# Kernel tuning notes

Measured on AMD Instinct MI355X. Metric: run time of the kernel, lower is better.

## Reference

```python
import jax, jax.numpy as jnp
import numpy as np

B, S, D, H, F = 4, 1024, 2048, 16, 8192
HD = D // H  # head dim = 128
EPS = 1e-5


def layer_norm(x, w, b):
    mu = jnp.mean(x, axis=-1, keepdims=True)
    var = jnp.mean(jnp.square(x - mu), axis=-1, keepdims=True)
    return (x - mu) * jax.lax.rsqrt(var + EPS) * w + b


def setup_inputs() -> dict:
    key = jax.random.key(0)
    ks = jax.random.split(key, 12)
    s = 0.02  # realistic init scale for weights
    return {
        "x": jax.random.normal(ks[0], (B, S, D), jnp.float32),
        "attention_mask": jnp.zeros((B, 1, 1, S), jnp.float32),
        "wq": jax.random.normal(ks[1], (D, D), jnp.float32) * s,
        "bq": jax.random.normal(ks[2], (D,), jnp.float32) * s,
        "wk": jax.random.normal(ks[3], (D, D), jnp.float32) * s,
        "bk": jax.random.normal(ks[4], (D,), jnp.float32) * s,
        "wv": jax.random.normal(ks[5], (D, D), jnp.float32) * s,
        "bv": jax.random.normal(ks[6], (D,), jnp.float32) * s,
        "wo": jax.random.normal(ks[7], (D, D), jnp.float32) * s,
        "bo": jax.random.normal(ks[8], (D,), jnp.float32) * s,
        "ln1_w": jnp.ones((D,), jnp.float32),
        "ln1_b": jnp.zeros((D,), jnp.float32),
        "wi": jax.random.normal(ks[9], (F, D), jnp.float32) * s,
        "bi": jax.random.normal(ks[10], (F,), jnp.float32) * s,
        "wo2": jax.random.normal(ks[11], (D, F), jnp.float32) * s,
        "bo2": jnp.zeros((D,), jnp.float32),
        "ln2_w": jnp.ones((D,), jnp.float32),
        "ln2_b": jnp.zeros((D,), jnp.float32),
    }


def reference(x, attention_mask, wq, bq, wk, bk, wv, bv, wo, bo,
              ln1_w, ln1_b, wi, bi, wo2, bo2, ln2_w, ln2_b):
    # --- self attention ---
    q = (jnp.einsum('bsd,ed->bse', x, wq) + bq).reshape(B, S, H, HD).transpose(0, 2, 1, 3)
    k = (jnp.einsum('bsd,ed->bse', x, wk) + bk).reshape(B, S, H, HD).transpose(0, 2, 1, 3)
    v = (jnp.einsum('bsd,ed->bse', x, wv) + bv).reshape(B, S, H, HD).transpose(0, 2, 1, 3)
    scores = jnp.einsum('bhqd,bhkd->bhqk', q, k) / jnp.sqrt(jnp.float32(HD))
    scores = scores + attention_mask  # additive mask, broadcast over heads/query
    probs = jax.nn.softmax(scores, axis=-1)
    ctx = jnp.einsum('bhqk,bhkd->bhqd', probs, v)
    ctx = ctx.transpose(0, 2, 1, 3).reshape(B, S, D)
    # --- attention output: dense + bias + residual + LayerNorm ---
    attn_out = layer_norm(jnp.einsum('bsd,ed->bse', ctx, wo) + bo + x, ln1_w, ln1_b)
    # --- FFN: intermediate dense + bias, GELU, output dense + bias + residual + LN ---
    inter = jnp.einsum('bsd,fd->bsf', attn_out, wi) + bi
    h = jax.nn.gelu(inter, approximate=False)
    out = layer_norm(jnp.einsum('bsf,df->bsd', h, wo2) + bo2 + attn_out, ln2_w, ln2_b)
    return out
```

## Files before the change

### kernel.cpp

```cpp
#include <hip/hip_runtime.h>
#include <hip/hip_bf16.h>
#include <cstdint>
#include <cstddef>

typedef __attribute__((ext_vector_type(8))) short short8;
typedef __attribute__((ext_vector_type(4))) float f32x4;

#define DEV static __device__ __forceinline__

constexpr int kS = 1024, kD = 2048, kH = 16, kHD = 128, kF = 8192;
constexpr int kM = 4096;
constexpr float kEPS = 1e-5f;

constexpr size_t SZ_DD   = (size_t)kD * kD * 2;
constexpr size_t SZ_FD   = (size_t)kF * kD * 2;
constexpr size_t SZ_MD16 = (size_t)kM * kD * 2;
constexpr size_t SZ_MD32 = (size_t)kM * kD * 4;
constexpr size_t OFF_WQ  = 0;
constexpr size_t OFF_WK  = OFF_WQ + SZ_DD;
constexpr size_t OFF_WV  = OFF_WK + SZ_DD;
constexpr size_t OFF_WO  = OFF_WV + SZ_DD;
constexpr size_t OFF_WI  = OFF_WO + SZ_DD;
constexpr size_t OFF_WO2 = OFF_WI + SZ_FD;
constexpr size_t OFF_XB  = OFF_WO2 + SZ_FD;
constexpr size_t OFF_Q   = OFF_XB + SZ_MD16;
constexpr size_t OFF_K   = OFF_Q + SZ_MD16;
constexpr size_t OFF_V   = OFF_K + SZ_MD16;
constexpr size_t OFF_H   = OFF_XB;
constexpr size_t OFF_CTX = OFF_V + SZ_MD16;
constexpr size_t OFF_Y1  = OFF_CTX + SZ_MD16;
constexpr size_t OFF_A1B = OFF_Y1 + SZ_MD32;
constexpr size_t OFF_Y2  = OFF_A1B + SZ_MD16;
constexpr size_t WS_NEED = OFF_Y2 + SZ_MD32;

DEV void gload16(const void* g, void* l) {
  __builtin_amdgcn_global_load_lds(
      (const __attribute__((address_space(1))) unsigned int*)g,
      (__attribute__((address_space(3))) unsigned int*)l, 16, 0, 0);
}

__global__ void cvt_bf16(const float* __restrict__ in, __hip_bfloat16* __restrict__ out, int n4) {
  int stride = gridDim.x * blockDim.x;
  for (int i = blockIdx.x * blockDim.x + threadIdx.x; i < n4; i += stride) {
    float4 v = reinterpret_cast<const float4*>(in)[i];
    union { ushort4 u; __hip_bfloat16 h[4]; } o;
    o.h[0] = __float2bfloat16(v.x);
    o.h[1] = __float2bfloat16(v.y);
    o.h[2] = __float2bfloat16(v.z);
    o.h[3] = __float2bfloat16(v.w);
    reinterpret_cast<ushort4*>(out)[i] = o.u;
  }
}

template <int MODE>
__global__ __launch_bounds__(512, 2)
void gemm256(const __hip_bfloat16* __restrict__ A,
             const __hip_bfloat16* __restrict__ Bt,
             const float* __restrict__ bias,
             float* __restrict__ out0, float* __restrict__ out1,
             void* __restrict__ outb,
             int M, int N, int K, int kLen) {
  __shared__ __align__(16) char lds[131072];
  const int tid = threadIdx.x;
  const int lane = tid & 63, w = tid >> 6;
  const int wm = w >> 2, wn = w & 3;
  const int lg = lane >> 4, lr = lane & 15;
  const int gy = M >> 8, gx = N >> 8;
  const int nwg = gridDim.x, orig = blockIdx.x;
  const int l = (orig & 7) * (nwg >> 3) + (orig >> 3);
  const int tilesPer = gx * gy;
  const int spl = l / tilesPer;
  const int rem = l - spl * tilesPer;
  const int bx = rem / gy, by = rem - bx * gy;
  const int m0 = by * 256, n0 = bx * 256;
  const int k0 = spl * kLen;
  const int NT = kLen >> 6;

  const char* gs[8];
  #pragma unroll
  for (int h = 0; h < 4; ++h) {
    const __hip_bfloat16* src = (h < 2) ? A : Bt;
    const int r0 = ((h < 2) ? m0 : n0) + (h & 1) * 128;
    #pragma unroll
    for (int i = 0; i < 2; ++i) {
      int c = i * 512 + tid;
      int row = c >> 3, slot = c & 7;
      gs[h * 2 + i] =
          (const char*)(src + (size_t)(r0 + row) * K + k0 + (slot ^ (row & 7)) * 8);
    }
  }

#define STAGE(P, H, TOFF)                                                          \
  {                                                                                \
    char* dstb = lds + (((H) < 2) ? 0 : 65536) + (P) * 32768 + ((H) & 1) * 16384;  \
    gload16(gs[(H) * 2 + 0] + (TOFF) * 128, dstb + (0 * 512 + tid) * 16);          \
    gload16(gs[(H) * 2 + 1] + (TOFF) * 128, dstb + (1 * 512 + tid) * 16);          \
  }

  auto ldA = [&](int P, int qm, int mr, int kk) {
    int row = qm * 128 + wm * 64 + mr * 16 + lr;
    return *reinterpret_cast<const short8*>(
        lds + P * 32768 + row * 128 + (((kk * 4 + lg) ^ (row & 7)) * 16));
  };
  auto ldB = [&](int P, int qn, int nr, int kk) {
    int row = qn * 128 + wn * 32 + nr * 16 + lr;
    return *reinterpret_cast<const short8*>(
        lds + 65536 + P * 32768 + row * 128 + (((kk * 4 + lg) ^ (row & 7)) * 16));
  };

  f32x4 acc[4][4][2] = {};

#define MFMA_QUAD(q)                                                            \
  __builtin_amdgcn_s_setprio(1);                                                \
  _Pragma("unroll")                                                             \
  for (int kk = 0; kk < 2; ++kk)                                                \
    _Pragma("unroll")                                                           \
    for (int mi = 0; mi < 4; ++mi)                                              \
      _Pragma("unroll")                                                         \
      for (int ni = 0; ni < 2; ++ni)                                            \
        acc[q][mi][ni] = __builtin_amdgcn_mfma_f32_16x16x32_bf16(               \
            av[kk][mi], bv[kk][ni], acc[q][mi][ni], 0, 0, 0);                   \
  __builtin_amdgcn_s_setprio(0);

#define TILE_BODY(P, PF)                                                        \
  {                                                                             \
                           \
    _Pragma("unroll")                                                           \
    for (int i = 0; i < 4; ++i) { av[0][i] = ldA(P, 0, i, 0); av[1][i] = ldA(P, 0, i, 1); } \
    _Pragma("unroll")                                                           \
    for (int i = 0; i < 2; ++i) { bv[0][i] = ldB(P, 0, i, 0); bv[1][i] = ldB(P, 0, i, 1); } \
    if (PF) STAGE((P) ^ 1, 0, 1 + (P));                                         \
    __builtin_amdgcn_s_barrier();                                               \
    asm volatile("s_waitcnt lgkmcnt(0)" ::: "memory");                          \
    __builtin_amdgcn_sched_barrier(0);                                          \
    MFMA_QUAD(0)                                                                \
    if (PF) { asm volatile("s_waitcnt vmcnt(4)" ::: "memory"); }                \
    else    { asm volatile("s_waitcnt vmcnt(2)" ::: "memory"); }                \
    __builtin_amdgcn_s_barrier();                                               \
                    \
    _Pragma("unroll")                                                           \
    for (int i = 0; i < 4; ++i) { av[0][i] = ldA(P, 1, i, 0); av[1][i] = ldA(P, 1, i, 1); } \
    if (PF) STAGE((P) ^ 1, 2, 1 + (P));                                         \
    __builtin_amdgcn_s_barrier();                                               \
    asm volatile("s_waitcnt lgkmcnt(0)" ::: "memory");                          \
    __builtin_amdgcn_sched_barrier(0);                                          \
    MFMA_QUAD(1)                                                                \
    if (PF) { asm volatile("s_waitcnt vmcnt(4)" ::: "memory"); }                \
    else    { asm volatile("s_waitcnt vmcnt(0)" ::: "memory"); }                \
    __builtin_amdgcn_s_barrier();                                               \
                    \
    _Pragma("unroll")                                                           \
    for (int i = 0; i < 2; ++i) { bv[0][i] = ldB(P, 1, i, 0); bv[1][i] = ldB(P, 1, i, 1); } \
    if (PF) STAGE((P) ^ 1, 1, 1 + (P));                                         \
    __builtin_amdgcn_s_barrier();                                               \
    asm volatile("s_waitcnt lgkmcnt(0)" ::: "memory");                          \
    __builtin_amdgcn_sched_barrier(0);                                          \
    MFMA_QUAD(2)                                                                \
    __builtin_amdgcn_s_barrier();                                               \
                 \
    _Pragma("unroll")                                                           \
    for (int i = 0; i < 4; ++i) { av[0][i] = ldA(P, 0, i, 0); av[1][i] = ldA(P, 0, i, 1); } \
    if (PF) STAGE((P) ^ 1, 3, 1 + (P));                                         \
    __builtin_amdgcn_s_barrier();                                               \
    asm volatile("s_waitcnt lgkmcnt(0)" ::: "memory");                          \
    __builtin_amdgcn_sched_barrier(0);                                          \
    MFMA_QUAD(3)                                                                \
    if (PF) { asm volatile("s_waitcnt vmcnt(4)" ::: "memory"); }                \
    __builtin_amdgcn_s_barrier();                                               \
  }

  STAGE(0, 0, 0) STAGE(0, 2, 0) STAGE(0, 1, 0) STAGE(0, 3, 0)
  asm volatile("s_waitcnt vmcnt(4)" ::: "memory");
  __builtin_amdgcn_s_barrier();

  for (int t2 = 0; t2 < NT; t2 += 2) {
    short8 av[2][4], bv[2][2];
    TILE_BODY(0, true)
    TILE_BODY(1, (t2 + 2 < NT))
    #pragma unroll
    for (int j = 0; j < 8; ++j) gs[j] += 256;
  }
#undef TILE_BODY
#undef MFMA_QUAD
#undef STAGE

  #pragma unroll
  for (int q = 0; q < 4; ++q) {
    const int qm = (q == 1 || q == 2) ? 1 : 0;
    const int qn = (q >= 2) ? 1 : 0;
    #pragma unroll
    for (int ni = 0; ni < 2; ++ni) {
      int col = n0 + qn * 128 + wn * 32 + ni * 16 + lr;
      float bvv = 0.f;
      if constexpr (MODE != 3) bvv = bias[col];
      #pragma unroll
      for (int mi = 0; mi < 4; ++mi) {
        int row0 = m0 + qm * 128 + wm * 64 + mi * 16 + lg * 4;
        #pragma unroll
        for (int r = 0; r < 4; ++r) {
          int row = row0 + r;
          float val = acc[q][mi][ni][r] + bvv;
          if constexpr (MODE == 0) {
            int which = col >> 11;
            int d = col & 2047;
            int hh = d >> 7, hd = d & 127;
            int bb = row >> 10, ss = row & 1023;
            __hip_bfloat16* base = (__hip_bfloat16*)outb + (size_t)which * ((size_t)kM * kD);
            if (which < 2)
              base[(((size_t)(bb * kH + hh)) * kS + ss) * kHD + hd] = __float2bfloat16(val);
            else
              base[(((size_t)(bb * kH + hh)) * kHD + hd) * kS + ss] = __float2bfloat16(val);
          } else if constexpr (MODE == 2) {
            float g = 0.5f * val * (1.0f + erff(val * 0.70710678118654752f));
            ((__hip_bfloat16*)outb)[(size_t)row * N + col] = __float2bfloat16(g);
          } else {
            float* o = spl ? out1 : out0;
            o[(size_t)row * N + col] = val;
          }
        }
      }
    }
  }
}

__global__ __launch_bounds__(512, 4)
void attn_fwd(const __hip_bfloat16* __restrict__ q,
              const __hip_bfloat16* __restrict__ k,
              const __hip_bfloat16* __restrict__ vt,
              const float* __restrict__ mask,
              __hip_bfloat16* __restrict__ ctx) {
  __shared__ __align__(16) char Ks[2][64 * 256];
  __shared__ __align__(16) char Vt[2][128 * 128];
  __shared__ __align__(16) char Ps[8][2048];
  const int tid = threadIdx.x, lane = tid & 63, w = tid >> 6;
  const int lg = lane >> 4, lr = lane & 15;
  const int orig = blockIdx.x;
  const int l = (orig & 7) * 64 + (orig >> 3);
  const int qt = l & 7, bh = l >> 3;
  const int b = bh >> 4;

  short8 qf[4];
  {
    const __hip_bfloat16* qp =
        q + ((size_t)bh * kS + qt * 128 + w * 16 + lr) * kHD + lg * 8;
    #pragma unroll
    for (int kk = 0; kk < 4; ++kk) qf[kk] = *reinterpret_cast<const short8*>(qp + kk * 32);
  }

  auto stage = [&](int bufi, int t) {
    #pragma unroll
    for (int i = 0; i < 2; ++i) {
      int c = i * 512 + tid;
      int row = c >> 4, slot = c & 15;
      gload16(k + ((size_t)bh * kS + t * 64 + row) * kHD + (slot ^ (row & 15)) * 8,
              Ks[bufi] + c * 16);
    }
    #pragma unroll
    for (int i = 0; i < 2; ++i) {
      int c = i * 512 + tid;
      int row = c >> 3, slot = c & 7;
      gload16(vt + ((size_t)bh * kHD + row) * kS + t * 64 + (slot ^ (row & 7)) * 8,
              Vt[bufi] + c * 16);
    }
  };

  f32x4 o[8] = {};
  float mrun[4], lrun[4];
  #pragma unroll
  for (int r = 0; r < 4; ++r) { mrun[r] = -1e30f; lrun[r] = 0.f; }
  const float scale = 0.08838834764831845f;

  stage(0, 0);
  __syncthreads();

  int buf = 0;
  for (int t = 0; t < 16; ++t) {
    if (t + 1 < 16) stage(buf ^ 1, t + 1);

    f32x4 sacc[4] = {};
    #pragma unroll
    for (int j = 0; j < 4; ++j) {
      int key = j * 16 + lr;
      #pragma unroll
      for (int kk = 0; kk < 4; ++kk) {
        short8 bfrag = *reinterpret_cast<const short8*>(
            Ks[buf] + key * 256 + (((kk * 4 + lg) ^ (key & 15)) * 16));
        sacc[j] = __builtin_amdgcn_mfma_f32_16x16x32_bf16(qf[kk], bfrag, sacc[j], 0, 0, 0);
      }
    }
    float sarr[4][4];
    #pragma unroll
    for (int j = 0; j < 4; ++j) {
      float mv = mask[(size_t)b * kS + t * 64 + j * 16 + lr];
      #pragma unroll
      for (int r = 0; r < 4; ++r) sarr[j][r] = sacc[j][r] * scale + mv;
    }
    #pragma unroll
    for (int r = 0; r < 4; ++r) {
      float tm = fmaxf(fmaxf(sarr[0][r], sarr[1][r]), fmaxf(sarr[2][r], sarr[3][r]));
      #pragma unroll
      for (int d = 1; d < 16; d <<= 1) tm = fmaxf(tm, __shfl_xor(tm, d));
      float mnew = fmaxf(mrun[r], tm);
      float alpha = __expf(mrun[r] - mnew);
      mrun[r] = mnew;
      float rs = 0.f;
      #pragma unroll
      for (int j = 0; j < 4; ++j) {
        float p = __expf(sarr[j][r] - mnew);
        sarr[j][r] = p;
        rs += p;
      }
      #pragma unroll
      for (int d = 1; d < 16; d <<= 1) rs += __shfl_xor(rs, d);
      lrun[r] = lrun[r] * alpha + rs;
      #pragma unroll
      for (int n = 0; n < 8; ++n) o[n][r] *= alpha;
    }
    #pragma unroll
    for (int r = 0; r < 4; ++r) {
      int qr = lg * 4 + r;
      #pragma unroll
      for (int j = 0; j < 4; ++j)
        *reinterpret_cast<__hip_bfloat16*>(
            Ps[w] + ((qr * 128 + (j * 16 + lr) * 2) ^ ((qr & 7) << 4))) =
            __float2bfloat16(sarr[j][r]);
    }
    #pragma unroll
    for (int kk2 = 0; kk2 < 2; ++kk2) {
      short8 pa = *reinterpret_cast<const short8*>(
          Ps[w] + ((lr * 128 + kk2 * 64 + lg * 16) ^ ((lr & 7) << 4)));
      #pragma unroll
      for (int n = 0; n < 8; ++n) {
        int hd = n * 16 + lr;
        short8 vb = *reinterpret_cast<const short8*>(
            Vt[buf] + hd * 128 + (((kk2 * 4 + lg) ^ (hd & 7)) * 16));
        o[n] = __builtin_amdgcn_mfma_f32_16x16x32_bf16(pa, vb, o[n], 0, 0, 0);
      }
    }
    __syncthreads();
    buf ^= 1;
  }

  const int h = bh & 15;
  #pragma unroll
  for (int r = 0; r < 4; ++r) {
    float inv = 1.0f / lrun[r];
    int srow = qt * 128 + w * 16 + lg * 4 + r;
    __hip_bfloat16* cp = ctx + ((size_t)b * kS + srow) * kD + h * 128 + lr;
    #pragma unroll
    for (int n = 0; n < 8; ++n) cp[n * 16] = __float2bfloat16(o[n][r] * inv);
  }
}

template <bool WB16>
__global__ void ln_fuse(const float* __restrict__ p0, const float* __restrict__ p1,
                        const float* __restrict__ bias, const float* __restrict__ res,
                        const float* __restrict__ w, const float* __restrict__ b,
                        float* __restrict__ outf, __hip_bfloat16* __restrict__ outb) {
  const int row = blockIdx.x, tid = threadIdx.x;
  const size_t base = (size_t)row * kD;
  float v[8];
  #pragma unroll
  for (int i = 0; i < 2; ++i) {
    int c4 = tid * 2 + i;
    float4 a  = reinterpret_cast<const float4*>(p0 + base)[c4];
    float4 bb = reinterpret_cast<const float4*>(p1 + base)[c4];
    float4 rr = reinterpret_cast<const float4*>(res + base)[c4];
    float4 bs = reinterpret_cast<const float4*>(bias)[c4];
    v[i * 4 + 0] = a.x + bb.x + rr.x + bs.x;
    v[i * 4 + 1] = a.y + bb.y + rr.y + bs.y;
    v[i * 4 + 2] = a.z + bb.z + rr.z + bs.z;
    v[i * 4 + 3] = a.w + bb.w + rr.w + bs.w;
  }
  float s = 0.f;
  #pragma unroll
  for (int i = 0; i < 8; ++i) s += v[i];
  #pragma unroll
  for (int off = 32; off > 0; off >>= 1) s += __shfl_down(s, off);
  __shared__ float r1[4], r2[4];
  if ((tid & 63) == 0) r1[tid >> 6] = s;
  __syncthreads();
  float mean = (r1[0] + r1[1] + r1[2] + r1[3]) * (1.0f / kD);
  float qv = 0.f;
  #pragma unroll
  for (int i = 0; i < 8; ++i) { float d = v[i] - mean; qv += d * d; }
  #pragma unroll
  for (int off = 32; off > 0; off >>= 1) qv += __shfl_down(qv, off);
  if ((tid & 63) == 0) r2[tid >> 6] = qv;
  __syncthreads();
  float rstd = rsqrtf((r2[0] + r2[1] + r2[2] + r2[3]) * (1.0f / kD) + kEPS);
  #pragma unroll
  for (int i = 0; i < 8; ++i) {
    int col = tid * 8 + i;
    float ov = (v[i] - mean) * rstd * w[col] + b[col];
    outf[base + col] = ov;
    if constexpr (WB16) outb[base + col] = __float2bfloat16(ov);
  }
}

extern "C" void kernel_launch(void* const* d_in, const int* in_sizes, int n_in,
                              void* d_out, int out_size, void* d_ws, size_t ws_size,
                              hipStream_t stream) {
  (void)in_sizes; (void)n_in; (void)out_size;
  if (ws_size < WS_NEED) return;
  const float* x    = (const float*)d_in[0];
  const float* mask = (const float*)d_in[1];
  const float* wq   = (const float*)d_in[2];
  const float* bq   = (const float*)d_in[3];
  const float* wk   = (const float*)d_in[4];
  const float* bk   = (const float*)d_in[5];
  const float* wv   = (const float*)d_in[6];
  const float* bv   = (const float*)d_in[7];
  const float* wo   = (const float*)d_in[8];
  const float* bo   = (const float*)d_in[9];
  const float* l1w  = (const float*)d_in[10];
  const float* l1b  = (const float*)d_in[11];
  const float* wi   = (const float*)d_in[12];
  const float* bi   = (const float*)d_in[13];
  const float* wo2  = (const float*)d_in[14];
  const float* bo2  = (const float*)d_in[15];
  const float* l2w  = (const float*)d_in[16];
  const float* l2b  = (const float*)d_in[17];

  char* ws = (char*)d_ws;
  __hip_bfloat16* wqb  = (__hip_bfloat16*)(ws + OFF_WQ);
  __hip_bfloat16* wkb  = (__hip_bfloat16*)(ws + OFF_WK);
  __hip_bfloat16* wvb  = (__hip_bfloat16*)(ws + OFF_WV);
  __hip_bfloat16* wob  = (__hip_bfloat16*)(ws + OFF_WO);
  __hip_bfloat16* wib  = (__hip_bfloat16*)(ws + OFF_WI);
  __hip_bfloat16* wo2b = (__hip_bfloat16*)(ws + OFF_WO2);
  __hip_bfloat16* xb   = (__hip_bfloat16*)(ws + OFF_XB);
  __hip_bfloat16* qb   = (__hip_bfloat16*)(ws + OFF_Q);
  __hip_bfloat16* kb2  = (__hip_bfloat16*)(ws + OFF_K);
  __hip_bfloat16* vtb  = (__hip_bfloat16*)(ws + OFF_V);
  __hip_bfloat16* hb   = (__hip_bfloat16*)(ws + OFF_H);
  __hip_bfloat16* ctxb = (__hip_bfloat16*)(ws + OFF_CTX);
  __hip_bfloat16* a1b  = (__hip_bfloat16*)(ws + OFF_A1B);
  float* y1   = (float*)(ws + OFF_Y1);
  float* y2   = (float*)(ws + OFF_Y2);
  float* f2p  = (float*)(ws + OFF_WQ);
  float* bqkv = (float*)(ws + OFF_Y2);

  cvt_bf16<<<2048, 256, 0, stream>>>(x,   xb,   kM * kD / 4);
  cvt_bf16<<<1024, 256, 0, stream>>>(wq,  wqb,  kD * kD / 4);
  cvt_bf16<<<1024, 256, 0, stream>>>(wk,  wkb,  kD * kD / 4);
  cvt_bf16<<<1024, 256, 0, stream>>>(wv,  wvb,  kD * kD / 4);
  cvt_bf16<<<1024, 256, 0, stream>>>(wo,  wob,  kD * kD / 4);
  cvt_bf16<<<2048, 256, 0, stream>>>(wi,  wib,  kF * kD / 4);
  cvt_bf16<<<2048, 256, 0, stream>>>(wo2, wo2b, kF * kD / 4);
  hipMemcpyAsync(bqkv,          bq, kD * 4, hipMemcpyDeviceToDevice, stream);
  hipMemcpyAsync(bqkv + kD,     bk, kD * 4, hipMemcpyDeviceToDevice, stream);
  hipMemcpyAsync(bqkv + 2 * kD, bv, kD * 4, hipMemcpyDeviceToDevice, stream);

  dim3 blk(512);
  gemm256<0><<<dim3(384), blk, 0, stream>>>(
      xb, wqb, bqkv, nullptr, nullptr, qb, kM, 6144, kD, kD);
  attn_fwd<<<dim3(512), dim3(512), 0, stream>>>(qb, kb2, vtb, mask, ctxb);
  gemm256<3><<<dim3(256), blk, 0, stream>>>(
      ctxb, wob, nullptr, y1, y2, nullptr, kM, kD, kD, kD / 2);
  ln_fuse<true><<<kM, 256, 0, stream>>>(y1, y2, bo, x, l1w, l1b, y1, a1b);
  gemm256<2><<<dim3(512), blk, 0, stream>>>(
      a1b, wib, bi, nullptr, nullptr, hb, kM, kF, kD, kD);
  gemm256<3><<<dim3(256), blk, 0, stream>>>(
      hb, wo2b, nullptr, y2, f2p, nullptr, kM, kD, kF, kF / 2);
  ln_fuse<false><<<kM, 256, 0, stream>>>(y2, f2p, bo2, y1, l2w, l2b, (float*)d_out, nullptr);
}
```

Before: 688.9 us.

## Reorder GEMM quadrant traversal and split MFMA waits to overlap LDS reads

```diff
diff --git a/kernel.cpp b/kernel.cpp
--- a/kernel.cpp
+++ b/kernel.cpp
@@ -110,68 +110,87 @@
 
   f32x4 acc[4][4][2] = {};
 
-#define MFMA_QUAD(q)                                                            \
-  __builtin_amdgcn_s_setprio(1);                                                \
+#define MFMA_HALF(q, kk)                                                        \
   _Pragma("unroll")                                                             \
-  for (int kk = 0; kk < 2; ++kk)                                                \
-    _Pragma("unroll")                                                           \
-    for (int mi = 0; mi < 4; ++mi)                                              \
-      _Pragma("unroll")                                                         \
-      for (int ni = 0; ni < 2; ++ni)                                            \
-        acc[q][mi][ni] = __builtin_amdgcn_mfma_f32_16x16x32_bf16(               \
-            av[kk][mi], bv[kk][ni], acc[q][mi][ni], 0, 0, 0);                   \
-  __builtin_amdgcn_s_setprio(0);
+  for (int mi = 0; mi < 4; ++mi)                                                \
+    _Pragma("unroll")                                                           \
+    for (int ni = 0; ni < 2; ++ni)                                              \
+      acc[q][mi][ni] = __builtin_amdgcn_mfma_f32_16x16x32_bf16(                 \
+          av[kk][mi], bv[kk][ni], acc[q][mi][ni], 0, 0, 0);
 
 #define TILE_BODY(P, PF)                                                        \
   {                                                                             \
-                           \
-    _Pragma("unroll")                                                           \
-    for (int i = 0; i < 4; ++i) { av[0][i] = ldA(P, 0, i, 0); av[1][i] = ldA(P, 0, i, 1); } \
-    _Pragma("unroll")                                                           \
-    for (int i = 0; i < 2; ++i) { bv[0][i] = ldB(P, 0, i, 0); bv[1][i] = ldB(P, 0, i, 1); } \
+            \
+    asm volatile("s_waitcnt vmcnt(4)" ::: "memory");                            \
+    __builtin_amdgcn_s_barrier();                                               \
+    _Pragma("unroll")                                                           \
+    for (int i = 0; i < 4; ++i) av[0][i] = ldA(P, 0, i, 0);                     \
+    _Pragma("unroll")                                                           \
+    for (int i = 0; i < 2; ++i) bv[0][i] = ldB(P, 0, i, 0);                     \
+    _Pragma("unroll")                                                           \
+    for (int i = 0; i < 4; ++i) av[1][i] = ldA(P, 0, i, 1);                     \
+    _Pragma("unroll")                                                           \
+    for (int i = 0; i < 2; ++i) bv[1][i] = ldB(P, 0, i, 1);                     \
     if (PF) STAGE((P) ^ 1, 0, 1 + (P));                                         \
-    __builtin_amdgcn_s_barrier();                                               \
+    asm volatile("s_waitcnt lgkmcnt(6)" ::: "memory");                          \
+    __builtin_amdgcn_sched_barrier(0);                                          \
+    __builtin_amdgcn_s_setprio(1);                                              \
+    MFMA_HALF(0, 0)                                                             \
     asm volatile("s_waitcnt lgkmcnt(0)" ::: "memory");                          \
     __builtin_amdgcn_sched_barrier(0);                                          \
-    MFMA_QUAD(0)                                                                \
+    MFMA_HALF(0, 1)                                                             \
+    __builtin_amdgcn_s_setprio(0);                                              \
+           \
     if (PF) { asm volatile("s_waitcnt vmcnt(4)" ::: "memory"); }                \
     else    { asm volatile("s_waitcnt vmcnt(2)" ::: "memory"); }                \
     __builtin_amdgcn_s_barrier();                                               \
-                    \
-    _Pragma("unroll")                                                           \
-    for (int i = 0; i < 4; ++i) { av[0][i] = ldA(P, 1, i, 0); av[1][i] = ldA(P, 1, i, 1); } \
+    _Pragma("unroll")                                                           \
+    for (int i = 0; i < 2; ++i) bv[0][i] = ldB(P, 1, i, 0);                     \
+    _Pragma("unroll")                                                           \
+    for (int i = 0; i < 2; ++i) bv[1][i] = ldB(P, 1, i, 1);                     \
     if (PF) STAGE((P) ^ 1, 2, 1 + (P));                                         \
-    __builtin_amdgcn_s_barrier();                                               \
+    asm volatile("s_waitcnt lgkmcnt(2)" ::: "memory");                          \
+    __builtin_amdgcn_sched_barrier(0);                                          \
+    __builtin_amdgcn_s_setprio(1);                                              \
+    MFMA_HALF(1, 0)                                                             \
     asm volatile("s_waitcnt lgkmcnt(0)" ::: "memory");                          \
     __builtin_amdgcn_sched_barrier(0);                                          \
-    MFMA_QUAD(1)                                                                \
+    MFMA_HALF(1, 1)                                                             \
+    __builtin_amdgcn_s_setprio(0);                                              \
+           \
     if (PF) { asm volatile("s_waitcnt vmcnt(4)" ::: "memory"); }                \
     else    { asm volatile("s_waitcnt vmcnt(0)" ::: "memory"); }                \
     __builtin_amdgcn_s_barrier();                                               \
-                    \
-    _Pragma("unroll")                                                           \
-    for (int i = 0; i < 2; ++i) { bv[0][i] = ldB(P, 1, i, 0); bv[1][i] = ldB(P, 1, i, 1); } \
+    _Pragma("unroll")                                                           \
+    for (int i = 0; i < 4; ++i) av[0][i] = ldA(P, 1, i, 0);                     \
+    _Pragma("unroll")                                                           \
+    for (int i = 0; i < 4; ++i) av[1][i] = ldA(P, 1, i, 1);                     \
+    if (PF) STAGE((P) ^ 1, 3, 1 + (P));                                         \
+    asm volatile("s_waitcnt lgkmcnt(4)" ::: "memory");                          \
+    __builtin_amdgcn_sched_barrier(0);                                          \
+    __builtin_amdgcn_s_setprio(1);                                              \
+    MFMA_HALF(2, 0)                                                             \
+    asm volatile("s_waitcnt lgkmcnt(0)" ::: "memory");                          \
+    __builtin_amdgcn_sched_barrier(0);                                          \
+    MFMA_HALF(2, 1)                                                             \
+    __builtin_amdgcn_s_setprio(0);                                              \
+     \
+    _Pragma("unroll")                                                           \
+    for (int i = 0; i < 2; ++i) bv[0][i] = ldB(P, 0, i, 0);                     \
+    _Pragma("unroll")                                                           \
+    for (int i = 0; i < 2; ++i) bv[1][i] = ldB(P, 0, i, 1);                     \
     if (PF) STAGE((P) ^ 1, 1, 1 + (P));                                         \
-    __builtin_amdgcn_s_barrier();                                               \
+    asm volatile("s_waitcnt lgkmcnt(2)" ::: "memory");                          \
+    __builtin_amdgcn_sched_barrier(0);                                          \
+    __builtin_amdgcn_s_setprio(1);                                              \
+    MFMA_HALF(3, 0)                                                             \
     asm volatile("s_waitcnt lgkmcnt(0)" ::: "memory");                          \
     __builtin_amdgcn_sched_barrier(0);                                          \
-    MFMA_QUAD(2)                                                                \
-    __builtin_amdgcn_s_barrier();                                               \
-                 \
-    _Pragma("unroll")                                                           \
-    for (int i = 0; i < 4; ++i) { av[0][i] = ldA(P, 0, i, 0); av[1][i] = ldA(P, 0, i, 1); } \
-    if (PF) STAGE((P) ^ 1, 3, 1 + (P));                                         \
-    __builtin_amdgcn_s_barrier();                                               \
-    asm volatile("s_waitcnt lgkmcnt(0)" ::: "memory");                          \
-    __builtin_amdgcn_sched_barrier(0);                                          \
-    MFMA_QUAD(3)                                                                \
-    if (PF) { asm volatile("s_waitcnt vmcnt(4)" ::: "memory"); }                \
-    __builtin_amdgcn_s_barrier();                                               \
-  }
-
-  STAGE(0, 0, 0) STAGE(0, 2, 0) STAGE(0, 1, 0) STAGE(0, 3, 0)
-  asm volatile("s_waitcnt vmcnt(4)" ::: "memory");
-  __builtin_amdgcn_s_barrier();
+    MFMA_HALF(3, 1)                                                             \
+    __builtin_amdgcn_s_setprio(0);                                              \
+  }
+
+  STAGE(0, 0, 0) STAGE(0, 2, 0) STAGE(0, 3, 0) STAGE(0, 1, 0)
 
   for (int t2 = 0; t2 < NT; t2 += 2) {
     short8 av[2][4], bv[2][2];
@@ -181,13 +200,13 @@
     for (int j = 0; j < 8; ++j) gs[j] += 256;
   }
 #undef TILE_BODY
-#undef MFMA_QUAD
+#undef MFMA_HALF
 #undef STAGE
 
   #pragma unroll
   for (int q = 0; q < 4; ++q) {
-    const int qm = (q == 1 || q == 2) ? 1 : 0;
-    const int qn = (q >= 2) ? 1 : 0;
+    const int qm = (q >= 2) ? 1 : 0;
+    const int qn = (q == 1 || q == 2) ? 1 : 0;
     #pragma unroll
     for (int ni = 0; ni < 2; ++ni) {
       int col = n0 + qn * 128 + wn * 32 + ni * 16 + lr;
```

After: 666.6 us. 3.2% less time.
